# Kernel tuning notes

Measured on AMD Instinct MI355X. Metric: run time of the kernel, lower is better.

Reference implementation:

```python
import jax, jax.numpy as jnp
import numpy as np
from jax import lax

EPS = 1e-12


def _conv_block(x, w, scale, bias, pool):
    # x: (N, Cin, H, W), w: (Cout, Cin, 3, 3). BN in eval mode folded into scale/bias.
    y = lax.conv_general_dilated(x, w, window_strides=(1, 1), padding='SAME',
                                 dimension_numbers=('NCHW', 'OIHW', 'NCHW'))
    y = y * scale[None, :, None, None] + bias[None, :, None, None]
    y = jax.nn.relu(y)
    if pool:
        y = lax.reduce_window(y, -jnp.inf, lax.max, (1, 1, 2, 2), (1, 1, 2, 2), 'VALID')
    return y


def _encoder(x, w1, s1, b1, w2, s2, b2, w3, s3, b3, w4, s4, b4):
    x = _conv_block(x, w1, s1, b1, True)
    x = _conv_block(x, w2, s2, b2, True)
    x = _conv_block(x, w3, s3, b3, False)
    x = _conv_block(x, w4, s4, b4, False)
    return x  # (N, 64, 21, 21)


def _l2norm(x, axis):
    n = jnp.sqrt(jnp.sum(x * x, axis=axis, keepdims=True))
    return x / jnp.maximum(n, EPS)


def setup_inputs() -> dict:
    key = jax.random.key(0)
    ks = jax.random.split(key, 8)
    B, NQ, Way, Shot, C, H, W = 2, 75, 5, 5, 3, 84, 84
    D = 64
    inp = {
        'query': jax.random.normal(ks[0], (B, NQ, C, H, W), jnp.float32),
        'support': jax.random.normal(ks[1], (B, Way, Shot, C, H, W), jnp.float32),
        'w1': jax.random.normal(ks[2], (D, C, 3, 3), jnp.float32) * 0.1,
        'w2': jax.random.normal(ks[3], (D, D, 3, 3), jnp.float32) * 0.05,
        'w3': jax.random.normal(ks[4], (D, D, 3, 3), jnp.float32) * 0.05,
        'w4': jax.random.normal(ks[5], (D, D, 3, 3), jnp.float32) * 0.05,
    }
    for i in range(1, 5):
        inp[f's{i}'] = jnp.ones((D,), jnp.float32)
        inp[f'b{i}'] = jnp.zeros((D,), jnp.float32)
    return inp


def reference(query, support, w1, s1, b1, w2, s2, b2, w3, s3, b3, w4, s4, b4):
    B, NQ, C, H, W = query.shape
    _, Way, Shot, _, _, _ = support.shape
    q_flat = query.reshape(B * NQ, C, H, W)
    s_flat = support.reshape(B * Way * Shot, C, H, W)
    q_feat = _encoder(q_flat, w1, s1, b1, w2, s2, b2, w3, s3, b3, w4, s4, b4)
    s_feat = _encoder(s_flat, w1, s1, b1, w2, s2, b2, w3, s3, b3, w4, s4, b4)
    D, h, w = q_feat.shape[1], q_feat.shape[2], q_feat.shape[3]
    HW = h * w
    q_local = _l2norm(q_feat.reshape(B, NQ, D, HW), axis=2)            # (B,NQ,D,HW)
    s_local = s_feat.reshape(B, Way, Shot, D, HW).mean(axis=2)          # mean over shots
    s_local = _l2norm(s_local, axis=2)                                  # (B,Way,D,HW)
    # all pairwise local cosine similarities, batched in one einsum
    sim = jnp.einsum('bqdm,bcdn->bqcmn', q_local, s_local)              # (B,NQ,Way,HW,HW)
    best = sim.max(axis=-1)                                             # best match per query descriptor
    scores = best.mean(axis=-1)                                         # (B,NQ,Way)
    return scores.reshape(B * NQ, Way)
```

## Files before the change

kernel.cpp:

```cpp
#include <hip/hip_runtime.h>

#define EPS 1e-12f

#define NIMG   200
#define NQIMG  150
#define BDIM   2
#define NQ     75
#define WAY    5
#define SHOT   5
#define DCH    64
#define H1     84
#define H2     42
#define H3     21
#define HW1    7056
#define HW2    1764
#define HW3    441
#define SST    448

#define W1_BLKS   8
#define W_BLKS    432

typedef __attribute__((ext_vector_type(8))) short bf16x8;
typedef __attribute__((ext_vector_type(4))) float f32x4;

__device__ __forceinline__ unsigned short f2bf(float f) {
    unsigned u = __float_as_uint(f);
    u += 0x7fffu + ((u >> 16) & 1u);
    return (unsigned short)(u >> 16);
}
__device__ __forceinline__ float bf2f(unsigned short h) {
    return __uint_as_float(((unsigned)h) << 16);
}
__device__ __forceinline__ int swz(int pix, int c) {
    return pix * 128 + ((c ^ ((pix >> 1) & 7)) << 4);
}

__global__ __launch_bounds__(256) void prep(
    const float* __restrict__ w1, const float* __restrict__ s1,
    const float* __restrict__ w2, const float* __restrict__ s2,
    const float* __restrict__ w3, const float* __restrict__ s3,
    const float* __restrict__ w4, const float* __restrict__ s4,
    unsigned short* __restrict__ p1, unsigned short* __restrict__ p2,
    unsigned short* __restrict__ p3, unsigned short* __restrict__ p4)
{
    int blk = blockIdx.x;
    if (blk < W1_BLKS) {
        int idx = blk * 256 + threadIdx.x;
        int j = idx & 7, lane = (idx >> 3) & 63, mt = idx >> 9;
        int co = (mt << 4) + (lane & 15);
        int k = ((lane >> 4) << 3) + j;
        float v = 0.f;
        if (k < 27) {
            int ci = k / 9, s = k % 9;
            v = w1[(co * 3 + ci) * 9 + s] * s1[co];
        }
        p1[idx] = f2bf(v);
    } else {
        int idx = (blk - W1_BLKS) * 256 + threadIdx.x;
        int which = idx / 36864;
        int r = idx % 36864;
        int j = r & 7, lane = (r >> 3) & 63, mt = (r >> 9) & 3, t = (r >> 11) & 1, s = r >> 12;
        int co = (mt << 4) + (lane & 15);
        int ci = (t << 5) + ((lane >> 4) << 3) + j;
        const float* w = (which == 0) ? w2 : (which == 1) ? w3 : w4;
        const float* sc = (which == 0) ? s2 : (which == 1) ? s3 : s4;
        unsigned short* p = (which == 0) ? p2 : (which == 1) ? p3 : p4;
        p[r] = f2bf(w[(co * 64 + ci) * 9 + s] * sc[co]);
    }
}

__global__ __launch_bounds__(256) void conv1_mfma(
    const float* __restrict__ qin, const float* __restrict__ sin_,
    const unsigned short* __restrict__ wp1,
    const float* __restrict__ bias,
    unsigned short* __restrict__ out)
{
    int img = blockIdx.x / 7, seg = blockIdx.x % 7;
    int tid = threadIdx.x;
    __shared__ unsigned short strip[3 * 14 * 86];

    const float* src = (img < NQIMG) ? (qin + (size_t)img * 3 * HW1)
                                     : (sin_ + (size_t)(img - NQIMG) * 3 * HW1);
    #pragma unroll
    for (int it = 0; it < 15; it++) {
        int i = it * 256 + tid;
        if (i < 3612) {
            int ci = i / 1204, rem = i % 1204;
            int r = rem / 86, xx = rem % 86;
            int y = 12 * seg + r - 1, x = xx - 1;
            float v = 0.f;
            if ((unsigned)y < (unsigned)H1 && (unsigned)x < (unsigned)H1)
                v = src[(size_t)ci * HW1 + y * H1 + x];
            strip[i] = f2bf(v);
        }
    }
    __syncthreads();

    int wv = tid >> 6, lane = tid & 63;
    int lc = lane & 15, kg = lane >> 4;

    const bf16x8* wvv = (const bf16x8*)wp1;
    bf16x8 a0 = wvv[lane];
    bf16x8 a1 = wvv[64 + lane];
    bf16x8 a2 = wvv[128 + lane];
    bf16x8 a3 = wvv[192 + lane];

    int off[8];
    #pragma unroll
    for (int j = 0; j < 8; j++) {
        int k = (kg << 3) + j;
        int kk = k < 27 ? k : 0;
        int ci = kk / 9, s = kk % 9;
        off[j] = ci * 1204 + (s / 3) * 86 + (s % 3);
    }

    f32x4 bini[4];
    #pragma unroll
    for (int mt = 0; mt < 4; mt++) {
        float4 bq = *reinterpret_cast<const float4*>(bias + (mt << 4) + (kg << 2));
        bini[mt] = (f32x4){bq.x, bq.y, bq.z, bq.w};
    }

    #pragma unroll
    for (int it = 0; it < 4; it++) {
        int pl = it * 64 + wv * 16 + lc;
        bool valid = pl < 252;
        int plc = valid ? pl : 251;
        int pyl = plc / 42, pxl = plc % 42;
        int base = pyl * 172 + 2 * pxl;

        bf16x8 b[4];
        #pragma unroll
        for (int j = 0; j < 8; j++) {
            int a = base + off[j];
            b[0][j] = (short)strip[a];
            b[1][j] = (short)strip[a + 1];
            b[2][j] = (short)strip[a + 86];
            b[3][j] = (short)strip[a + 87];
        }

        f32x4 acc[4][4];
        #pragma unroll
        for (int mt = 0; mt < 4; mt++)
            #pragma unroll
            for (int sub = 0; sub < 4; sub++)
                acc[mt][sub] = bini[mt];
        #pragma unroll
        for (int sub = 0; sub < 4; sub++) {
            acc[0][sub] = __builtin_amdgcn_mfma_f32_16x16x32_bf16(a0, b[sub], acc[0][sub], 0, 0, 0);
            acc[1][sub] = __builtin_amdgcn_mfma_f32_16x16x32_bf16(a1, b[sub], acc[1][sub], 0, 0, 0);
            acc[2][sub] = __builtin_amdgcn_mfma_f32_16x16x32_bf16(a2, b[sub], acc[2][sub], 0, 0, 0);
            acc[3][sub] = __builtin_amdgcn_mfma_f32_16x16x32_bf16(a3, b[sub], acc[3][sub], 0, 0, 0);
        }

        if (valid) {
            int p = seg * 252 + pl;
            #pragma unroll
            for (int mt = 0; mt < 4; mt++) {
                unsigned short uo[4];
                #pragma unroll
                for (int r = 0; r < 4; r++) {
                    float m = fmaxf(fmaxf(acc[mt][0][r], acc[mt][1][r]),
                                    fmaxf(acc[mt][2][r], acc[mt][3][r]));
                    uo[r] = f2bf(fmaxf(m, 0.f));
                }
                uint2 pk;
                pk.x = (unsigned)uo[0] | ((unsigned)uo[1] << 16);
                pk.y = (unsigned)uo[2] | ((unsigned)uo[3] << 16);
                *reinterpret_cast<uint2*>(out + ((size_t)img * HW2 + p) * DCH + (mt << 4) + (kg << 2)) = pk;
            }
        }
    }
}

__global__ __launch_bounds__(256) void conv2_mfma_pool(
    const unsigned short* __restrict__ act,
    const unsigned short* __restrict__ wp,
    const float* __restrict__ bias,
    unsigned short* __restrict__ out)
{
    int img = blockIdx.x / 7, tg = blockIdx.x % 7;
    int tid = threadIdx.x;
    __shared__ unsigned short lds[8 * 44 * DCH];

    const unsigned short* ab = act + (size_t)img * HW2 * DCH;
    int ybase = 6 * tg - 1;
    #pragma unroll
    for (int it = 0; it < 11; it++) {
        int idx = it * 256 + tid;
        int pix = idx >> 3, c = idx & 7;
        int r = pix / 44, xx = pix % 44;
        int y = ybase + r, x = xx - 1;
        bf16x8 v = (bf16x8)(short)0;
        if ((unsigned)y < (unsigned)H2 && (unsigned)x < (unsigned)H2)
            v = *(const bf16x8*)(ab + ((size_t)(y * H2 + x)) * DCH + (c << 3));
        *(bf16x8*)((char*)lds + swz(pix, c)) = v;
    }
    __syncthreads();

    int wv = tid >> 6, lane = tid & 63;
    int lc = lane & 15, kg = lane >> 4;
    int p_local = wv * 16 + lc;
    bool valid = p_local < 63;
    int pl = valid ? p_local : 62;
    int pyl = pl / 21, pxl = pl % 21;
    int pixc[4];
    #pragma unroll
    for (int sub = 0; sub < 4; sub++)
        pixc[sub] = (2 * pyl + (sub >> 1) + 1) * 44 + (2 * pxl + (sub & 1) + 1);

    f32x4 bini[4];
    #pragma unroll
    for (int mt = 0; mt < 4; mt++) {
        float4 bq = *reinterpret_cast<const float4*>(bias + (mt << 4) + (kg << 2));
        bini[mt] = (f32x4){bq.x, bq.y, bq.z, bq.w};
    }

    const bf16x8* wvv = (const bf16x8*)wp;
    f32x4 acc[4][4];
    #pragma unroll
    for (int i = 0; i < 4; i++)
        #pragma unroll
        for (int j = 0; j < 4; j++)
            acc[i][j] = bini[i];

    for (int s = 0; s < 9; s++) {
        int offs = (s / 3 - 1) * 44 + (s % 3 - 1);
        #pragma unroll
        for (int t = 0; t < 2; t++) {
            int fbase = ((s * 2 + t) * 4) << 6;
            bf16x8 a0 = wvv[fbase + lane];
            bf16x8 a1 = wvv[fbase + 64 + lane];
            bf16x8 a2 = wvv[fbase + 128 + lane];
            bf16x8 a3 = wvv[fbase + 192 + lane];
            int c = (t << 2) + kg;
            bf16x8 b[4];
            #pragma unroll
            for (int sub = 0; sub < 4; sub++) {
                int pix = pixc[sub] + offs;
                b[sub] = *(const bf16x8*)((const char*)lds + swz(pix, c));
            }
            #pragma unroll
            for (int sub = 0; sub < 4; sub++) {
                acc[0][sub] = __builtin_amdgcn_mfma_f32_16x16x32_bf16(a0, b[sub], acc[0][sub], 0, 0, 0);
                acc[1][sub] = __builtin_amdgcn_mfma_f32_16x16x32_bf16(a1, b[sub], acc[1][sub], 0, 0, 0);
                acc[2][sub] = __builtin_amdgcn_mfma_f32_16x16x32_bf16(a2, b[sub], acc[2][sub], 0, 0, 0);
                acc[3][sub] = __builtin_amdgcn_mfma_f32_16x16x32_bf16(a3, b[sub], acc[3][sub], 0, 0, 0);
            }
        }
    }

    if (!valid) return;
    int p = tg * 63 + p_local;
    #pragma unroll
    for (int mt = 0; mt < 4; mt++) {
        unsigned short uo[4];
        #pragma unroll
        for (int r = 0; r < 4; r++) {
            float m = fmaxf(fmaxf(acc[mt][0][r], acc[mt][1][r]),
                            fmaxf(acc[mt][2][r], acc[mt][3][r]));
            uo[r] = f2bf(fmaxf(m, 0.f));
        }
        uint2 pk;
        pk.x = (unsigned)uo[0] | ((unsigned)uo[1] << 16);
        pk.y = (unsigned)uo[2] | ((unsigned)uo[3] << 16);
        *reinterpret_cast<uint2*>(out + ((size_t)img * HW3 + p) * DCH + (mt << 4) + (kg << 2)) = pk;
    }
}

__global__ __launch_bounds__(256) void conv34_fused(
    const unsigned short* __restrict__ act,
    const unsigned short* __restrict__ wp3, const unsigned short* __restrict__ wp4,
    const float* __restrict__ b3, const float* __restrict__ b4,
    unsigned short* __restrict__ a4out,
    unsigned short* __restrict__ qlout)
{
    int img = blockIdx.x;
    int tid = threadIdx.x;
    __shared__ unsigned short lds[529 * DCH];

    const unsigned short* ab = act + (size_t)img * HW3 * DCH;
    #pragma unroll
    for (int it = 0; it < 17; it++) {
        int idx = it * 256 + tid;
        if (idx < 529 * 8) {
            int pix = idx >> 3, c = idx & 7;
            int r = pix / 23, xx = pix % 23;
            int y = r - 1, x = xx - 1;
            bf16x8 v = (bf16x8)(short)0;
            if ((unsigned)y < (unsigned)H3 && (unsigned)x < (unsigned)H3)
                v = *(const bf16x8*)(ab + ((size_t)(y * H3 + x)) * DCH + (c << 3));
            *(bf16x8*)((char*)lds + swz(pix, c)) = v;
        }
    }
    __syncthreads();

    int wv = tid >> 6, lane = tid & 63;
    int lc = lane & 15, kg = lane >> 4;
    int pixBase[7];
    bool pv[7];
    #pragma unroll
    for (int i = 0; i < 7; i++) {
        int p = (wv * 7 + i) * 16 + lc;
        pv[i] = p < HW3;
        int pc = pv[i] ? p : HW3 - 1;
        pixBase[i] = (pc / 21) * 23 + (pc % 21);
    }

    f32x4 bini[4];
    #pragma unroll
    for (int mt = 0; mt < 4; mt++) {
        float4 bq = *reinterpret_cast<const float4*>(b3 + (mt << 4) + (kg << 2));
        bini[mt] = (f32x4){bq.x, bq.y, bq.z, bq.w};
    }

    f32x4 acc[7][4];
    #pragma unroll
    for (int i = 0; i < 7; i++)
        #pragma unroll
        for (int m = 0; m < 4; m++)
            acc[i][m] = bini[m];

    const bf16x8* wv3 = (const bf16x8*)wp3;
    for (int s = 0; s < 9; s++) {
        int offs = (s / 3) * 23 + (s % 3);
        #pragma unroll
        for (int t = 0; t < 2; t++) {
            int fbase = ((s * 2 + t) * 4) << 6;
            bf16x8 a0 = wv3[fbase + lane];
            bf16x8 a1 = wv3[fbase + 64 + lane];
            bf16x8 a2 = wv3[fbase + 128 + lane];
            bf16x8 a3 = wv3[fbase + 192 + lane];
            int c = (t << 2) + kg;
            #pragma unroll
            for (int i = 0; i < 7; i++) {
                int pix = pixBase[i] + offs;
                bf16x8 bb = *(const bf16x8*)((const char*)lds + swz(pix, c));
                acc[i][0] = __builtin_amdgcn_mfma_f32_16x16x32_bf16(a0, bb, acc[i][0], 0, 0, 0);
                acc[i][1] = __builtin_amdgcn_mfma_f32_16x16x32_bf16(a1, bb, acc[i][1], 0, 0, 0);
                acc[i][2] = __builtin_amdgcn_mfma_f32_16x16x32_bf16(a2, bb, acc[i][2], 0, 0, 0);
                acc[i][3] = __builtin_amdgcn_mfma_f32_16x16x32_bf16(a3, bb, acc[i][3], 0, 0, 0);
            }
        }
    }

    __syncthreads();

    #pragma unroll
    for (int i = 0; i < 7; i++) {
        if (!pv[i]) continue;
        int pix = pixBase[i] + 24;
        #pragma unroll
        for (int mt = 0; mt < 4; mt++) {
            unsigned short uo[4];
            #pragma unroll
            for (int r = 0; r < 4; r++)
                uo[r] = f2bf(fmaxf(acc[i][mt][r], 0.f));
            uint2 pk;
            pk.x = (unsigned)uo[0] | ((unsigned)uo[1] << 16);
            pk.y = (unsigned)uo[2] | ((unsigned)uo[3] << 16);
            int c = (mt << 1) + (kg >> 1);
            *(uint2*)((char*)lds + swz(pix, c) + ((kg & 1) << 3)) = pk;
        }
    }
    #pragma unroll
    for (int it = 0; it < 3; it++) {
        int idx = it * 256 + tid;
        if (idx < 704) {
            int j = idx >> 3, c = idx & 7;
            int pix;
            if (j < 23)      pix = j;
            else if (j < 46) pix = 506 + (j - 23);
            else { int k = j - 46; pix = (1 + (k >> 1)) * 23 + (k & 1) * 22; }
            *(bf16x8*)((char*)lds + swz(pix, c)) = (bf16x8)(short)0;
        }
    }
    __syncthreads();

    #pragma unroll
    for (int mt = 0; mt < 4; mt++) {
        float4 bq = *reinterpret_cast<const float4*>(b4 + (mt << 4) + (kg << 2));
        bini[mt] = (f32x4){bq.x, bq.y, bq.z, bq.w};
    }
    #pragma unroll
    for (int i = 0; i < 7; i++)
        #pragma unroll
        for (int m = 0; m < 4; m++)
            acc[i][m] = bini[m];

    const bf16x8* wv4 = (const bf16x8*)wp4;
    for (int s = 0; s < 9; s++) {
        int offs = (s / 3) * 23 + (s % 3);
        #pragma unroll
        for (int t = 0; t < 2; t++) {
            int fbase = ((s * 2 + t) * 4) << 6;
            bf16x8 a0 = wv4[fbase + lane];
            bf16x8 a1 = wv4[fbase + 64 + lane];
            bf16x8 a2 = wv4[fbase + 128 + lane];
            bf16x8 a3 = wv4[fbase + 192 + lane];
            int c = (t << 2) + kg;
            #pragma unroll
            for (int i = 0; i < 7; i++) {
                int pix = pixBase[i] + offs;
                bf16x8 bb = *(const bf16x8*)((const char*)lds + swz(pix, c));
                acc[i][0] = __builtin_amdgcn_mfma_f32_16x16x32_bf16(a0, bb, acc[i][0], 0, 0, 0);
                acc[i][1] = __builtin_amdgcn_mfma_f32_16x16x32_bf16(a1, bb, acc[i][1], 0, 0, 0);
                acc[i][2] = __builtin_amdgcn_mfma_f32_16x16x32_bf16(a2, bb, acc[i][2], 0, 0, 0);
                acc[i][3] = __builtin_amdgcn_mfma_f32_16x16x32_bf16(a3, bb, acc[i][3], 0, 0, 0);
            }
        }
    }

    if (img < NQIMG) {
        #pragma unroll
        for (int i = 0; i < 7; i++) {
            float v[4][4];
            float ssq = 0.f;
            #pragma unroll
            for (int mt = 0; mt < 4; mt++)
                #pragma unroll
                for (int r = 0; r < 4; r++) {
                    float x = fmaxf(acc[i][mt][r], 0.f);
                    v[mt][r] = x;
                    ssq = fmaf(x, x, ssq);
                }
            ssq += __shfl_xor(ssq, 16, 64);
            ssq += __shfl_xor(ssq, 32, 64);
            float inv = 1.f / fmaxf(sqrtf(ssq), EPS);
            if (!pv[i]) continue;
            int p = (wv * 7 + i) * 16 + lc;
            #pragma unroll
            for (int mt = 0; mt < 4; mt++) {
                unsigned short uo[4];
                #pragma unroll
                for (int r = 0; r < 4; r++)
                    uo[r] = f2bf(v[mt][r] * inv);
                uint2 pk;
                pk.x = (unsigned)uo[0] | ((unsigned)uo[1] << 16);
                pk.y = (unsigned)uo[2] | ((unsigned)uo[3] << 16);
                *reinterpret_cast<uint2*>(qlout + ((size_t)img * HW3 + p) * DCH + (mt << 4) + (kg << 2)) = pk;
            }
        }
    } else {
        #pragma unroll
        for (int mt = 0; mt < 4; mt++) {
            #pragma unroll
            for (int i = 0; i < 7; i++) {
                if (!pv[i]) continue;
                int p = (wv * 7 + i) * 16 + lc;
                unsigned short uo[4];
                #pragma unroll
                for (int r = 0; r < 4; r++)
                    uo[r] = f2bf(fmaxf(acc[i][mt][r], 0.f));
                uint2 pk;
                pk.x = (unsigned)uo[0] | ((unsigned)uo[1] << 16);
                pk.y = (unsigned)uo[2] | ((unsigned)uo[3] << 16);
                *reinterpret_cast<uint2*>(a4out + ((size_t)img * HW3 + p) * DCH + (mt << 4) + (kg << 2)) = pk;
            }
        }
    }
}

__global__ __launch_bounds__(256) void s_mean_norm(
    const unsigned short* __restrict__ feat, unsigned short* __restrict__ s_local)
{
    int idx = blockIdx.x * 256 + threadIdx.x;
    if (idx >= BDIM * WAY * SST) return;
    int hw = idx % SST;
    int bc = idx / SST;
    bf16x8* o = (bf16x8*)(s_local + (size_t)idx * DCH);
    if (hw >= HW3) {
        #pragma unroll
        for (int g = 0; g < 8; g++) o[g] = (bf16x8)(short)0;
        return;
    }
    int img0 = NQIMG + bc * SHOT;
    float v[DCH];
    #pragma unroll
    for (int d = 0; d < DCH; d++) v[d] = 0.f;
    for (int sh = 0; sh < SHOT; sh++) {
        const bf16x8* f = (const bf16x8*)(feat + ((size_t)(img0 + sh) * HW3 + hw) * DCH);
        #pragma unroll
        for (int g = 0; g < 8; g++) {
            bf16x8 x = f[g];
            #pragma unroll
            for (int j = 0; j < 8; j++)
                v[g * 8 + j] += bf2f((unsigned short)x[j]);
        }
    }
    float ss = 0.f;
    #pragma unroll
    for (int d = 0; d < DCH; d++) {
        v[d] *= (1.f / SHOT);
        ss = fmaf(v[d], v[d], ss);
    }
    float inv = 1.f / fmaxf(sqrtf(ss), EPS);
    #pragma unroll
    for (int g = 0; g < 8; g++) {
        bf16x8 pk;
        #pragma unroll
        for (int j = 0; j < 8; j++) pk[j] = (short)f2bf(v[g * 8 + j] * inv);
        o[g] = pk;
    }
}

__global__ __launch_bounds__(256) void sim_mfma(
    const unsigned short* __restrict__ qloc,
    const unsigned short* __restrict__ sloc,
    float* __restrict__ out)
{
    int blk = blockIdx.x;
    int imgq = blk / WAY, way = blk % WAY;
    int b = imgq / NQ;
    const unsigned short* qp = qloc + (size_t)imgq * HW3 * DCH;
    const unsigned short* sp = sloc + (size_t)(b * WAY + way) * SST * DCH;

    int tid = threadIdx.x;
    int wv = tid >> 6, lane = tid & 63;
    int lc = lane & 15, kg = lane >> 4;
    int mt0 = wv * 7;

    bf16x8 qa0[7], qa1[7];
    #pragma unroll
    for (int i = 0; i < 7; i++) {
        const unsigned short* qrow = qp + (size_t)((mt0 + i) * 16 + lc) * DCH + (kg << 3);
        qa0[i] = *(const bf16x8*)(qrow);
        qa1[i] = *(const bf16x8*)(qrow + 32);
    }
    f32x4 rmax[7];
    #pragma unroll
    for (int i = 0; i < 7; i++)
        rmax[i] = (f32x4){-1e30f, -1e30f, -1e30f, -1e30f};

    const f32x4 z4 = (f32x4){0.f, 0.f, 0.f, 0.f};
    const unsigned short* sbase = sp + (size_t)lc * DCH + (kg << 3);

    for (int g = 0; g < 6; g++) {
        bf16x8 s0[4], s1[4];
        #pragma unroll
        for (int u = 0; u < 4; u++) {
            const unsigned short* r0 = sbase + (size_t)(4 * g + u) * 16 * DCH;
            s0[u] = *(const bf16x8*)(r0);
            s1[u] = *(const bf16x8*)(r0 + 32);
        }
        #pragma unroll
        for (int i = 0; i < 7; i++) {
            f32x4 a[4];
            #pragma unroll
            for (int u = 0; u < 4; u++) {
                a[u] = __builtin_amdgcn_mfma_f32_16x16x32_bf16(qa0[i], s0[u], z4, 0, 0, 0);
                a[u] = __builtin_amdgcn_mfma_f32_16x16x32_bf16(qa1[i], s1[u], a[u], 0, 0, 0);
            }
            #pragma unroll
            for (int r = 0; r < 4; r++)
                rmax[i][r] = fmaxf(rmax[i][r],
                                   fmaxf(fmaxf(a[0][r], a[1][r]), fmaxf(a[2][r], a[3][r])));
        }
    }
    {
        bf16x8 s0[4], s1[4];
        #pragma unroll
        for (int u = 0; u < 4; u++) {
            const unsigned short* r0 = sbase + (size_t)(24 + u) * 16 * DCH;
            s0[u] = *(const bf16x8*)(r0);
            s1[u] = *(const bf16x8*)(r0 + 32);
        }
        bool nval = (432 + lc) < HW3;
        #pragma unroll
        for (int i = 0; i < 7; i++) {
            f32x4 a[4];
            #pragma unroll
            for (int u = 0; u < 4; u++) {
                a[u] = __builtin_amdgcn_mfma_f32_16x16x32_bf16(qa0[i], s0[u], z4, 0, 0, 0);
                a[u] = __builtin_amdgcn_mfma_f32_16x16x32_bf16(qa1[i], s1[u], a[u], 0, 0, 0);
            }
            #pragma unroll
            for (int r = 0; r < 4; r++)
                rmax[i][r] = fmaxf(rmax[i][r],
                                   fmaxf(fmaxf(a[0][r], a[1][r]),
                                         fmaxf(a[2][r], nval ? a[3][r] : -1e30f)));
        }
    }

    float msum = 0.f;
    #pragma unroll
    for (int i = 0; i < 7; i++) {
        #pragma unroll
        for (int r = 0; r < 4; r++) {
            float v = rmax[i][r];
            v = fmaxf(v, __shfl_xor(v, 1, 64));
            v = fmaxf(v, __shfl_xor(v, 2, 64));
            v = fmaxf(v, __shfl_xor(v, 4, 64));
            v = fmaxf(v, __shfl_xor(v, 8, 64));
            int m = (mt0 + i) * 16 + (kg << 2) + r;
            if (lc == 0 && m < HW3) msum += v;
        }
    }
    #pragma unroll
    for (int off = 32; off > 0; off >>= 1)
        msum += __shfl_xor(msum, off, 64);
    __shared__ float red[4];
    if (lane == 0) red[wv] = msum;
    __syncthreads();
    if (tid == 0)
        out[(size_t)imgq * WAY + way] = (red[0] + red[1] + red[2] + red[3]) * (1.f / HW3);
}

extern "C" void kernel_launch(void* const* d_in, const int* in_sizes, int n_in,
                              void* d_out, int out_size, void* d_ws, size_t ws_size,
                              hipStream_t stream) {
    const float* query   = (const float*)d_in[0];
    const float* support = (const float*)d_in[1];
    const float* w1 = (const float*)d_in[2];
    const float* w2 = (const float*)d_in[3];
    const float* w3 = (const float*)d_in[4];
    const float* w4 = (const float*)d_in[5];
    const float* s1 = (const float*)d_in[6];
    const float* b1 = (const float*)d_in[7];
    const float* s2 = (const float*)d_in[8];
    const float* b2 = (const float*)d_in[9];
    const float* s3 = (const float*)d_in[10];
    const float* b3 = (const float*)d_in[11];
    const float* s4 = (const float*)d_in[12];
    const float* b4 = (const float*)d_in[13];
    float* out = (float*)d_out;

    char* ws = (char*)d_ws;
    unsigned short* A1  = (unsigned short*)(ws);
    unsigned short* A2  = (unsigned short*)(ws + 45158400);
    unsigned short* A4  = (unsigned short*)(ws + 56448000);
    unsigned short* QL  = (unsigned short*)(ws + 67737600);
    unsigned short* SL  = (unsigned short*)(ws + 76204800);
    unsigned short* WP2 = (unsigned short*)(ws + 76778240);
    unsigned short* WP3 = (unsigned short*)(ws + 76851968);
    unsigned short* WP4 = (unsigned short*)(ws + 76925696);
    unsigned short* WP1 = (unsigned short*)(ws + 76999424);

    prep<<<W1_BLKS + W_BLKS, 256, 0, stream>>>(
        w1, s1, w2, s2, w3, s3, w4, s4, WP1, WP2, WP3, WP4);

    conv1_mfma<<<NIMG * 7, 256, 0, stream>>>(query, support, WP1, b1, A1);
    conv2_mfma_pool<<<NIMG * 7, 256, 0, stream>>>(A1, WP2, b2, A2);
    conv34_fused<<<NIMG, 256, 0, stream>>>(A2, WP3, WP4, b3, b4, A4, QL);

    s_mean_norm<<<(BDIM * WAY * SST + 255) / 256, 256, 0, stream>>>(A4, SL);

    sim_mfma<<<NQIMG * WAY, 256, 0, stream>>>(QL, SL, out);
}
```

Measured before the change: 142.6 us.

## Fuse conv1 and conv2 via LDS halo strip, pre-pad input to bf16

Conv1 (with pooling) and conv2 (with pooling) now run in one kernel. Each block recomputes the conv1 output rows it needs, including a one-row halo, and keeps them in LDS, so the 45 MB A1 intermediate never goes through global memory. A new pre-pass in prep turns the fp32 inputs into a zero-padded bf16 layout, which lets the strip load use aligned 32-bit reads. The cost is some recomputed conv1 halo rows, more LDS per block (which may lower occupancy), and an extra full pass over the input in prep.

```diff
diff --git a/kernel.cpp b/kernel.cpp
--- a/kernel.cpp
+++ b/kernel.cpp
@@ -15,8 +15,11 @@
 #define HW1    7056
 #define HW2    1764
 #define HW3    441
+#define PH     86
+#define PSZ    7396
 #define SST    448
 
+#define PAD_BLKS  17335
 #define W1_BLKS   8
 #define W_BLKS    432
 
@@ -36,16 +39,32 @@
 }
 
 __global__ __launch_bounds__(256) void prep(
+    const float* __restrict__ qin, const float* __restrict__ sin_,
     const float* __restrict__ w1, const float* __restrict__ s1,
     const float* __restrict__ w2, const float* __restrict__ s2,
     const float* __restrict__ w3, const float* __restrict__ s3,
     const float* __restrict__ w4, const float* __restrict__ s4,
-    unsigned short* __restrict__ p1, unsigned short* __restrict__ p2,
-    unsigned short* __restrict__ p3, unsigned short* __restrict__ p4)
+    unsigned short* __restrict__ pad, unsigned short* __restrict__ p1,
+    unsigned short* __restrict__ p2, unsigned short* __restrict__ p3,
+    unsigned short* __restrict__ p4)
 {
     int blk = blockIdx.x;
-    if (blk < W1_BLKS) {
+    if (blk < PAD_BLKS) {
         int idx = blk * 256 + threadIdx.x;
+        if (idx >= NIMG * 3 * PSZ) return;
+        int img = idx / (3 * PSZ);
+        int rem = idx % (3 * PSZ);
+        int ci = rem / PSZ, p = rem % PSZ;
+        int iy = p / PH, ix = p % PH;
+        float v = 0.f;
+        if (iy >= 1 && iy <= H1 && ix >= 1 && ix <= H1) {
+            const float* src = (img < NQIMG) ? (qin + (size_t)img * 3 * HW1)
+                                             : (sin_ + (size_t)(img - NQIMG) * 3 * HW1);
+            v = src[(size_t)ci * HW1 + (iy - 1) * H1 + (ix - 1)];
+        }
+        pad[idx] = f2bf(v);
+    } else if (blk < PAD_BLKS + W1_BLKS) {
+        int idx = (blk - PAD_BLKS) * 256 + threadIdx.x;
         int j = idx & 7, lane = (idx >> 3) & 63, mt = idx >> 9;
         int co = (mt << 4) + (lane & 15);
         int k = ((lane >> 4) << 3) + j;
@@ -56,7 +75,7 @@
         }
         p1[idx] = f2bf(v);
     } else {
-        int idx = (blk - W1_BLKS) * 256 + threadIdx.x;
+        int idx = (blk - PAD_BLKS - W1_BLKS) * 256 + threadIdx.x;
         int which = idx / 36864;
         int r = idx % 36864;
         int j = r & 7, lane = (r >> 3) & 63, mt = (r >> 9) & 3, t = (r >> 11) & 1, s = r >> 12;
@@ -69,137 +88,118 @@
     }
 }
 
-__global__ __launch_bounds__(256) void conv1_mfma(
-    const float* __restrict__ qin, const float* __restrict__ sin_,
-    const unsigned short* __restrict__ wp1,
-    const float* __restrict__ bias,
-    unsigned short* __restrict__ out)
-{
-    int img = blockIdx.x / 7, seg = blockIdx.x % 7;
-    int tid = threadIdx.x;
-    __shared__ unsigned short strip[3 * 14 * 86];
-
-    const float* src = (img < NQIMG) ? (qin + (size_t)img * 3 * HW1)
-                                     : (sin_ + (size_t)(img - NQIMG) * 3 * HW1);
-    #pragma unroll
-    for (int it = 0; it < 15; it++) {
-        int i = it * 256 + tid;
-        if (i < 3612) {
-            int ci = i / 1204, rem = i % 1204;
-            int r = rem / 86, xx = rem % 86;
-            int y = 12 * seg + r - 1, x = xx - 1;
-            float v = 0.f;
-            if ((unsigned)y < (unsigned)H1 && (unsigned)x < (unsigned)H1)
-                v = src[(size_t)ci * HW1 + y * H1 + x];
-            strip[i] = f2bf(v);
-        }
-    }
-    __syncthreads();
-
-    int wv = tid >> 6, lane = tid & 63;
-    int lc = lane & 15, kg = lane >> 4;
-
-    const bf16x8* wvv = (const bf16x8*)wp1;
-    bf16x8 a0 = wvv[lane];
-    bf16x8 a1 = wvv[64 + lane];
-    bf16x8 a2 = wvv[128 + lane];
-    bf16x8 a3 = wvv[192 + lane];
-
-    int off[8];
-    #pragma unroll
-    for (int j = 0; j < 8; j++) {
-        int k = (kg << 3) + j;
-        int kk = k < 27 ? k : 0;
-        int ci = kk / 9, s = kk % 9;
-        off[j] = ci * 1204 + (s / 3) * 86 + (s % 3);
-    }
-
-    f32x4 bini[4];
-    #pragma unroll
-    for (int mt = 0; mt < 4; mt++) {
-        float4 bq = *reinterpret_cast<const float4*>(bias + (mt << 4) + (kg << 2));
-        bini[mt] = (f32x4){bq.x, bq.y, bq.z, bq.w};
-    }
-
-    #pragma unroll
-    for (int it = 0; it < 4; it++) {
-        int pl = it * 64 + wv * 16 + lc;
-        bool valid = pl < 252;
-        int plc = valid ? pl : 251;
-        int pyl = plc / 42, pxl = plc % 42;
-        int base = pyl * 172 + 2 * pxl;
-
-        bf16x8 b[4];
-        #pragma unroll
-        for (int j = 0; j < 8; j++) {
-            int a = base + off[j];
-            b[0][j] = (short)strip[a];
-            b[1][j] = (short)strip[a + 1];
-            b[2][j] = (short)strip[a + 86];
-            b[3][j] = (short)strip[a + 87];
-        }
-
-        f32x4 acc[4][4];
-        #pragma unroll
-        for (int mt = 0; mt < 4; mt++)
-            #pragma unroll
-            for (int sub = 0; sub < 4; sub++)
-                acc[mt][sub] = bini[mt];
-        #pragma unroll
-        for (int sub = 0; sub < 4; sub++) {
-            acc[0][sub] = __builtin_amdgcn_mfma_f32_16x16x32_bf16(a0, b[sub], acc[0][sub], 0, 0, 0);
-            acc[1][sub] = __builtin_amdgcn_mfma_f32_16x16x32_bf16(a1, b[sub], acc[1][sub], 0, 0, 0);
-            acc[2][sub] = __builtin_amdgcn_mfma_f32_16x16x32_bf16(a2, b[sub], acc[2][sub], 0, 0, 0);
-            acc[3][sub] = __builtin_amdgcn_mfma_f32_16x16x32_bf16(a3, b[sub], acc[3][sub], 0, 0, 0);
-        }
-
-        if (valid) {
-            int p = seg * 252 + pl;
-            #pragma unroll
-            for (int mt = 0; mt < 4; mt++) {
-                unsigned short uo[4];
-                #pragma unroll
-                for (int r = 0; r < 4; r++) {
-                    float m = fmaxf(fmaxf(acc[mt][0][r], acc[mt][1][r]),
-                                    fmaxf(acc[mt][2][r], acc[mt][3][r]));
-                    uo[r] = f2bf(fmaxf(m, 0.f));
-                }
-                uint2 pk;
-                pk.x = (unsigned)uo[0] | ((unsigned)uo[1] << 16);
-                pk.y = (unsigned)uo[2] | ((unsigned)uo[3] << 16);
-                *reinterpret_cast<uint2*>(out + ((size_t)img * HW2 + p) * DCH + (mt << 4) + (kg << 2)) = pk;
-            }
-        }
-    }
-}
-
-__global__ __launch_bounds__(256) void conv2_mfma_pool(
-    const unsigned short* __restrict__ act,
-    const unsigned short* __restrict__ wp,
-    const float* __restrict__ bias,
+__global__ __launch_bounds__(256) void conv12_fused(
+    const unsigned short* __restrict__ pad,
+    const unsigned short* __restrict__ wp1, const float* __restrict__ bias1,
+    const unsigned short* __restrict__ wp2, const float* __restrict__ bias2,
     unsigned short* __restrict__ out)
 {
     int img = blockIdx.x / 7, tg = blockIdx.x % 7;
     int tid = threadIdx.x;
-    __shared__ unsigned short lds[8 * 44 * DCH];
-
-    const unsigned short* ab = act + (size_t)img * HW2 * DCH;
-    int ybase = 6 * tg - 1;
-    #pragma unroll
-    for (int it = 0; it < 11; it++) {
-        int idx = it * 256 + tid;
-        int pix = idx >> 3, c = idx & 7;
-        int r = pix / 44, xx = pix % 44;
-        int y = ybase + r, x = xx - 1;
-        bf16x8 v = (bf16x8)(short)0;
-        if ((unsigned)y < (unsigned)H2 && (unsigned)x < (unsigned)H2)
-            v = *(const bf16x8*)(ab + ((size_t)(y * H2 + x)) * DCH + (c << 3));
-        *(bf16x8*)((char*)lds + swz(pix, c)) = v;
+    __shared__ __attribute__((aligned(16))) unsigned short strip[3 * 18 * 86];
+    __shared__ unsigned short lds2[352 * DCH];
+
+    const unsigned* srcd = (const unsigned*)pad;
+    size_t ibase = (size_t)img * 3 * (PSZ / 2);
+    #pragma unroll
+    for (int it = 0; it < 10; it++) {
+        int i = it * 256 + tid;
+        if (i < 2322) {
+            int ci = i / 774, rem = i % 774;
+            int sr = rem / 43, d = rem % 43;
+            int y = 12 * tg - 3 + sr;
+            unsigned v = 0;
+            if (y >= -1 && y <= 84)
+                v = srcd[ibase + ci * 3698 + (y + 1) * 43 + d];
+            ((unsigned*)strip)[ci * 774 + sr * 43 + d] = v;
+        }
     }
     __syncthreads();
 
     int wv = tid >> 6, lane = tid & 63;
     int lc = lane & 15, kg = lane >> 4;
+
+    {
+        const bf16x8* w1v = (const bf16x8*)wp1;
+        bf16x8 a0 = w1v[lane];
+        bf16x8 a1 = w1v[64 + lane];
+        bf16x8 a2 = w1v[128 + lane];
+        bf16x8 a3 = w1v[192 + lane];
+
+        int off[8];
+        #pragma unroll
+        for (int j = 0; j < 8; j++) {
+            int k = (kg << 3) + j;
+            int kk = k < 27 ? k : 0;
+            int ci = kk / 9, s = kk % 9;
+            off[j] = ci * 1548 + (s / 3) * 86 + (s % 3);
+        }
+
+        f32x4 bini[4];
+        #pragma unroll
+        for (int mt = 0; mt < 4; mt++) {
+            float4 bq = *reinterpret_cast<const float4*>(bias1 + (mt << 4) + (kg << 2));
+            bini[mt] = (f32x4){bq.x, bq.y, bq.z, bq.w};
+        }
+
+        #pragma unroll
+        for (int rnd = 0; rnd < 6; rnd++) {
+            int pl = rnd * 64 + wv * 16 + lc;
+            bool instrip = pl < 352;
+            int plc = instrip ? pl : 0;
+            int rr = plc / 44, cc = plc % 44;
+            int pr = 6 * tg - 1 + rr, pc = cc - 1;
+            bool validpx = instrip && ((unsigned)pr < (unsigned)H2) && ((unsigned)pc < (unsigned)H2);
+            int ccc = ((unsigned)pc < (unsigned)H2) ? cc : 1;
+            int base = (2 * rr) * 86 + (2 * ccc - 2);
+
+            bf16x8 b[4];
+            #pragma unroll
+            for (int j = 0; j < 8; j++) {
+                int a = base + off[j];
+                b[0][j] = (short)strip[a];
+                b[1][j] = (short)strip[a + 1];
+                b[2][j] = (short)strip[a + 86];
+                b[3][j] = (short)strip[a + 87];
+            }
+
+            f32x4 acc[4][4];
+            #pragma unroll
+            for (int mt = 0; mt < 4; mt++)
+                #pragma unroll
+                for (int sub = 0; sub < 4; sub++)
+                    acc[mt][sub] = bini[mt];
+            #pragma unroll
+            for (int sub = 0; sub < 4; sub++) {
+                acc[0][sub] = __builtin_amdgcn_mfma_f32_16x16x32_bf16(a0, b[sub], acc[0][sub], 0, 0, 0);
+                acc[1][sub] = __builtin_amdgcn_mfma_f32_16x16x32_bf16(a1, b[sub], acc[1][sub], 0, 0, 0);
+                acc[2][sub] = __builtin_amdgcn_mfma_f32_16x16x32_bf16(a2, b[sub], acc[2][sub], 0, 0, 0);
+                acc[3][sub] = __builtin_amdgcn_mfma_f32_16x16x32_bf16(a3, b[sub], acc[3][sub], 0, 0, 0);
+            }
+
+            if (instrip) {
+                #pragma unroll
+                for (int mt = 0; mt < 4; mt++) {
+                    uint2 pk = make_uint2(0u, 0u);
+                    if (validpx) {
+                        unsigned short uo[4];
+                        #pragma unroll
+                        for (int r = 0; r < 4; r++) {
+                            float m = fmaxf(fmaxf(acc[mt][0][r], acc[mt][1][r]),
+                                            fmaxf(acc[mt][2][r], acc[mt][3][r]));
+                            uo[r] = f2bf(fmaxf(m, 0.f));
+                        }
+                        pk.x = (unsigned)uo[0] | ((unsigned)uo[1] << 16);
+                        pk.y = (unsigned)uo[2] | ((unsigned)uo[3] << 16);
+                    }
+                    int c = (mt << 1) + (kg >> 1);
+                    *(uint2*)((char*)lds2 + swz(pl, c) + ((kg & 1) << 3)) = pk;
+                }
+            }
+        }
+    }
+    __syncthreads();
+
     int p_local = wv * 16 + lc;
     bool valid = p_local < 63;
     int pl = valid ? p_local : 62;
@@ -212,11 +212,11 @@
     f32x4 bini[4];
     #pragma unroll
     for (int mt = 0; mt < 4; mt++) {
-        float4 bq = *reinterpret_cast<const float4*>(bias + (mt << 4) + (kg << 2));
+        float4 bq = *reinterpret_cast<const float4*>(bias2 + (mt << 4) + (kg << 2));
         bini[mt] = (f32x4){bq.x, bq.y, bq.z, bq.w};
     }
 
-    const bf16x8* wvv = (const bf16x8*)wp;
+    const bf16x8* wvv = (const bf16x8*)wp2;
     f32x4 acc[4][4];
     #pragma unroll
     for (int i = 0; i < 4; i++)
@@ -238,7 +238,7 @@
             #pragma unroll
             for (int sub = 0; sub < 4; sub++) {
                 int pix = pixc[sub] + offs;
-                b[sub] = *(const bf16x8*)((const char*)lds + swz(pix, c));
+                b[sub] = *(const bf16x8*)((const char*)lds2 + swz(pix, c));
             }
             #pragma unroll
             for (int sub = 0; sub < 4; sub++) {
@@ -626,21 +626,20 @@
     float* out = (float*)d_out;
 
     char* ws = (char*)d_ws;
-    unsigned short* A1  = (unsigned short*)(ws);
-    unsigned short* A2  = (unsigned short*)(ws + 45158400);
-    unsigned short* A4  = (unsigned short*)(ws + 56448000);
-    unsigned short* QL  = (unsigned short*)(ws + 67737600);
-    unsigned short* SL  = (unsigned short*)(ws + 76204800);
-    unsigned short* WP2 = (unsigned short*)(ws + 76778240);
-    unsigned short* WP3 = (unsigned short*)(ws + 76851968);
-    unsigned short* WP4 = (unsigned short*)(ws + 76925696);
-    unsigned short* WP1 = (unsigned short*)(ws + 76999424);
-
-    prep<<<W1_BLKS + W_BLKS, 256, 0, stream>>>(
-        w1, s1, w2, s2, w3, s3, w4, s4, WP1, WP2, WP3, WP4);
-
-    conv1_mfma<<<NIMG * 7, 256, 0, stream>>>(query, support, WP1, b1, A1);
-    conv2_mfma_pool<<<NIMG * 7, 256, 0, stream>>>(A1, WP2, b2, A2);
+    unsigned short* A2  = (unsigned short*)(ws);
+    unsigned short* A4  = (unsigned short*)(ws + 11289600);
+    unsigned short* QL  = (unsigned short*)(ws + 22579200);
+    unsigned short* SL  = (unsigned short*)(ws + 31046400);
+    unsigned short* WP2 = (unsigned short*)(ws + 31619840);
+    unsigned short* WP3 = (unsigned short*)(ws + 31693568);
+    unsigned short* WP4 = (unsigned short*)(ws + 31767296);
+    unsigned short* WP1 = (unsigned short*)(ws + 31841024);
+    unsigned short* PAD = (unsigned short*)(ws + 31845120);
+
+    prep<<<PAD_BLKS + W1_BLKS + W_BLKS, 256, 0, stream>>>(
+        query, support, w1, s1, w2, s2, w3, s3, w4, s4, PAD, WP1, WP2, WP3, WP4);
+
+    conv12_fused<<<NIMG * 7, 256, 0, stream>>>(PAD, WP1, b1, WP2, b2, A2);
     conv34_fused<<<NIMG, 256, 0, stream>>>(A2, WP3, WP4, b3, b4, A4, QL);
 
     s_mean_norm<<<(BDIM * WAY * SST + 255) / 256, 256, 0, stream>>>(A4, SL);
```

New measurement: 139.9 us. Within noise of the previous version (-1.9%).
